# Optimization experiments

Hardware: AMD Instinct MI355X
Metric: run time of the kernel (lower is better)

## Reference

```python
import jax, jax.numpy as jnp
import numpy as np


def setup_inputs() -> dict:
    key = jax.random.key(0)
    k1, k2, k3, k4, k5, k6 = jax.random.split(key, 6)
    B, N = 256, 512
    return {
        "node_features": jax.random.normal(k1, (B, N, 2), dtype=jnp.float32),
        "adj_matrices": jax.random.uniform(k2, (B, N, N), dtype=jnp.float32),
        "W1": jax.random.normal(k3, (2, 4), dtype=jnp.float32) * 0.5,
        "b1": jax.random.normal(k4, (4,), dtype=jnp.float32) * 0.1,
        "W2": jax.random.normal(k5, (4, 1), dtype=jnp.float32) * 0.5,
        "b2": jax.random.normal(k6, (1,), dtype=jnp.float32) * 0.1,
    }


def reference(node_features, adj_matrices, W1, b1, W2, b2):
    # GraphConv (1 layer): aggregate neighbors via dense adjacency, linear, ReLU
    agg = jnp.einsum('bnm,bmf->bnf', adj_matrices, node_features)   # [B,N,2]
    h = jax.nn.relu(agg @ W1 + b1)                                   # [B,N,4]
    # dense readout + sum over nodes
    prop = h @ W2 + b2                                               # [B,N,1]
    return jnp.sum(prop, axis=1)                                     # [B,1]
```

## Files before the change

### kernel.cpp

```cpp
#include <hip/hip_runtime.h>

#define BATCH 256
#define NNODE 512

typedef float floatx4 __attribute__((ext_vector_type(4)));

__global__ void init_out_kernel(const float* __restrict__ b2, float* __restrict__ out) {
    int i = blockIdx.x * blockDim.x + threadIdx.x;
    if (i < BATCH) out[i] = (float)NNODE * b2[0];
}

__global__ __launch_bounds__(256, 4) void gcn_main_kernel(
    const float* __restrict__ x,
    const float* __restrict__ adj,
    const float* __restrict__ W1,
    const float* __restrict__ b1,
    const float* __restrict__ W2,
    float* __restrict__ out)
{
    __shared__ __align__(16) float sx0[NNODE];
    __shared__ __align__(16) float sx1[NNODE];
    __shared__ float swsum[4];

    const int b     = blockIdx.x >> 3;
    const int chunk = blockIdx.x & 7;
    const int t     = threadIdx.x;

    {
        const float4 v = ((const float4*)(x + (size_t)b * NNODE * 2))[t];
        const int m = 2 * t;
        sx0[m]     = v.x; sx1[m]     = v.y;
        sx0[m + 1] = v.z; sx1[m + 1] = v.w;
    }

    float w1[8], bb1[4], w2[4];
#pragma unroll
    for (int j = 0; j < 8; ++j) w1[j] = W1[j];
#pragma unroll
    for (int j = 0; j < 4; ++j) { bb1[j] = b1[j]; w2[j] = W2[j]; }

    __syncthreads();

    const int wave = t >> 6;
    const int lane = t & 63;
    const int sub  = lane >> 4;
    const int l    = lane & 15;

    const int row0 = chunk * 64 + wave * 16 + sub * 4;
    const floatx4* __restrict__ arow =
        (const floatx4*)(adj + ((size_t)b * NNODE + row0) * NNODE);

    float s0[4] = {0.f, 0.f, 0.f, 0.f};
    float s1[4] = {0.f, 0.f, 0.f, 0.f};

#pragma unroll
    for (int k = 0; k < 8; ++k) {
        const int c = l + k * 16;
        const floatx4 xv0 = ((const floatx4*)sx0)[c];
        const floatx4 xv1 = ((const floatx4*)sx1)[c];
#pragma unroll
        for (int r = 0; r < 4; ++r) {
            const floatx4 av = __builtin_nontemporal_load(&arow[(size_t)r * (NNODE / 4) + c]);
            s0[r] += av.x * xv0.x + av.y * xv0.y + av.z * xv0.z + av.w * xv0.w;
            s1[r] += av.x * xv1.x + av.y * xv1.y + av.z * xv1.z + av.w * xv1.w;
        }
    }

#pragma unroll
    for (int m = 1; m < 16; m <<= 1) {
#pragma unroll
        for (int r = 0; r < 4; ++r) {
            s0[r] += __shfl_xor(s0[r], m, 64);
            s1[r] += __shfl_xor(s1[r], m, 64);
        }
    }

    float acc = 0.0f;
    if (l == 0) {
#pragma unroll
        for (int r = 0; r < 4; ++r) {
            float p = 0.0f;
#pragma unroll
            for (int j = 0; j < 4; ++j) {
                float h = fmaf(s0[r], w1[j], fmaf(s1[r], w1[4 + j], bb1[j]));
                h = fmaxf(h, 0.0f);
                p += h * w2[j];
            }
            acc += p;
        }
    }

#pragma unroll
    for (int m = 1; m < 64; m <<= 1) acc += __shfl_xor(acc, m, 64);
    if (lane == 0) swsum[wave] = acc;
    __syncthreads();
    if (t == 0) {
        atomicAdd(out + b, swsum[0] + swsum[1] + swsum[2] + swsum[3]);
    }
}

extern "C" void kernel_launch(void* const* d_in, const int* in_sizes, int n_in,
                              void* d_out, int out_size, void* d_ws, size_t ws_size,
                              hipStream_t stream) {
    const float* x   = (const float*)d_in[0];
    const float* adj = (const float*)d_in[1];
    const float* W1  = (const float*)d_in[2];
    const float* b1  = (const float*)d_in[3];
    const float* W2  = (const float*)d_in[4];
    const float* b2  = (const float*)d_in[5];
    float* out = (float*)d_out;

    hipLaunchKernelGGL(init_out_kernel, dim3(1), dim3(256), 0, stream, b2, out);
    hipLaunchKernelGGL(gcn_main_kernel, dim3(BATCH * 8), dim3(256), 0, stream,
                       x, adj, W1, b1, W2, out);
}
```

Baseline: 347.1 us.

## Map whole wave to each adjacency row and hoist x vectors into registers

Each wave now handles 16 full rows, with every lane loading two float4 columns per row, instead of splitting rows across 16-lane subgroups. The x feature vectors are loaded from shared memory into registers once rather than on every iteration. This removes repeated LDS reads but adds a full 64-lane butterfly reduction for 32 accumulators. That means many more shuffles and more register pressure. Every lane then computes the MLP redundantly, so the final cross-lane reduction is dropped.

```diff
diff --git a/kernel.cpp b/kernel.cpp
--- a/kernel.cpp
+++ b/kernel.cpp
@@ -2,6 +2,7 @@
 
 #define BATCH 256
 #define NNODE 512
+#define RPW 16
 
 typedef float floatx4 __attribute__((ext_vector_type(4)));
 
@@ -43,55 +44,50 @@
 
     const int wave = t >> 6;
     const int lane = t & 63;
-    const int sub  = lane >> 4;
-    const int l    = lane & 15;
 
-    const int row0 = chunk * 64 + wave * 16 + sub * 4;
+    const floatx4* sx0v = (const floatx4*)sx0;
+    const floatx4* sx1v = (const floatx4*)sx1;
+    const int c0 = lane, c1 = lane + 64;
+    const floatx4 x0a = sx0v[c0], x1a = sx1v[c0];
+    const floatx4 x0b = sx0v[c1], x1b = sx1v[c1];
+
+    const int row0 = chunk * 64 + wave * RPW;
     const floatx4* __restrict__ arow =
         (const floatx4*)(adj + ((size_t)b * NNODE + row0) * NNODE);
 
-    float s0[4] = {0.f, 0.f, 0.f, 0.f};
-    float s1[4] = {0.f, 0.f, 0.f, 0.f};
-
+    float s0[RPW], s1[RPW];
 #pragma unroll
-    for (int k = 0; k < 8; ++k) {
-        const int c = l + k * 16;
-        const floatx4 xv0 = ((const floatx4*)sx0)[c];
-        const floatx4 xv1 = ((const floatx4*)sx1)[c];
-#pragma unroll
-        for (int r = 0; r < 4; ++r) {
-            const floatx4 av = __builtin_nontemporal_load(&arow[(size_t)r * (NNODE / 4) + c]);
-            s0[r] += av.x * xv0.x + av.y * xv0.y + av.z * xv0.z + av.w * xv0.w;
-            s1[r] += av.x * xv1.x + av.y * xv1.y + av.z * xv1.z + av.w * xv1.w;
-        }
+    for (int r = 0; r < RPW; ++r) {
+        const floatx4 a0 = __builtin_nontemporal_load(&arow[(size_t)r * (NNODE / 4) + c0]);
+        const floatx4 a1 = __builtin_nontemporal_load(&arow[(size_t)r * (NNODE / 4) + c1]);
+        s0[r] = a0.x * x0a.x + a0.y * x0a.y + a0.z * x0a.z + a0.w * x0a.w
+              + a1.x * x0b.x + a1.y * x0b.y + a1.z * x0b.z + a1.w * x0b.w;
+        s1[r] = a0.x * x1a.x + a0.y * x1a.y + a0.z * x1a.z + a0.w * x1a.w
+              + a1.x * x1b.x + a1.y * x1b.y + a1.z * x1b.z + a1.w * x1b.w;
     }
 
 #pragma unroll
-    for (int m = 1; m < 16; m <<= 1) {
+    for (int m = 1; m < 64; m <<= 1) {
 #pragma unroll
-        for (int r = 0; r < 4; ++r) {
+        for (int r = 0; r < RPW; ++r) {
             s0[r] += __shfl_xor(s0[r], m, 64);
             s1[r] += __shfl_xor(s1[r], m, 64);
         }
     }
 
     float acc = 0.0f;
-    if (l == 0) {
 #pragma unroll
-        for (int r = 0; r < 4; ++r) {
-            float p = 0.0f;
+    for (int r = 0; r < RPW; ++r) {
+        float p = 0.0f;
 #pragma unroll
-            for (int j = 0; j < 4; ++j) {
-                float h = fmaf(s0[r], w1[j], fmaf(s1[r], w1[4 + j], bb1[j]));
-                h = fmaxf(h, 0.0f);
-                p += h * w2[j];
-            }
-            acc += p;
+        for (int j = 0; j < 4; ++j) {
+            float h = fmaf(s0[r], w1[j], fmaf(s1[r], w1[4 + j], bb1[j]));
+            h = fmaxf(h, 0.0f);
+            p = fmaf(h, w2[j], p);
         }
+        acc += p;
     }
 
-#pragma unroll
-    for (int m = 1; m < 64; m <<= 1) acc += __shfl_xor(acc, m, 64);
     if (lane == 0) swsum[wave] = acc;
     __syncthreads();
     if (t == 0) {
```

Result: no change. 342.8 us (-1.2%).
